# Performance work log

Hardware: AMD Instinct MI355X
Metric: run time of the kernel (lower is better)

## Reference

```python
import jax, jax.numpy as jnp
import numpy as np

EPS = 1e-12  # torch F.normalize eps

def _normalize(x):
    n = jnp.sqrt(jnp.sum(x * x, axis=-1, keepdims=True))
    return x / jnp.maximum(n, EPS)

def bgs_extended(d6s):
    # d6s: [B, N, D, 3, 2] -> rotation [B, N, D, 3, 3] (columns b1,b2,b3)
    b1 = _normalize(d6s[..., :, 0])
    a2 = d6s[..., :, 1]
    dot = jnp.sum(b1 * a2, axis=-1, keepdims=True)
    b2 = _normalize(a2 - dot * b1)
    b3 = jnp.cross(b1, b2, axis=-1)
    return jnp.stack([b1, b2, b3], axis=-1)

def setup_inputs() -> dict:
    key = jax.random.key(0)
    k1, k2, k3, k4, k5 = jax.random.split(key, 5)
    B, N, D, F = 8, 8192, 64, 64
    X = jax.random.normal(k1, (B, N, D, 3), dtype=jnp.float32)
    J = jax.random.normal(k2, (B, N, D, 3, 2), dtype=jnp.float32)
    A = jax.random.normal(k3, (F, D), dtype=jnp.float32)
    Bm = jax.random.normal(k4, (F, D), dtype=jnp.float32)
    C = jax.random.normal(k5, (F, D), dtype=jnp.float32)
    return {"X": X, "J": J, "A": A, "Bm": Bm, "C": C}

def reference(X, J, A, Bm, C):
    R = bgs_extended(J)  # [B,N,D,3,3]
    # RT_i X = dot(column i of R, X) -> compute all three at once: [B,N,D,3]
    RTX = jnp.einsum('bndki,bndk->bndi', R, X)
    rt0, rt1, rt2 = RTX[..., 0:1], RTX[..., 1:2], RTX[..., 2:3]
    # get_rrtx(i, R, s) == R[..., :, i] * s
    a_term = R[..., :, 0] * rt0 + R[..., :, 1] * rt1
    b_term = R[..., :, 1] * rt0 - R[..., :, 0] * rt1
    c_term = R[..., :, 2] * rt2
    Y = (jnp.einsum('fe,bnei->bnfi', A, a_term)
         + jnp.einsum('fe,bnei->bnfi', Bm, b_term)
         + jnp.einsum('fe,bnei->bnfi', C, c_term))
    return Y
```

## Files before the change

kernel.cpp:

```cpp
#include <hip/hip_runtime.h>

typedef __bf16 bf16;
typedef bf16 bf16x8 __attribute__((ext_vector_type(8)));
typedef float f32x4 __attribute__((ext_vector_type(4)));
typedef unsigned int u32;

#define PTS 16
#define WREG 6144

__device__ __forceinline__ void gld_lds16(const void* g, void* l) {
    __builtin_amdgcn_global_load_lds(
        (const __attribute__((address_space(1))) u32*)g,
        (__attribute__((address_space(3))) u32*)l, 16, 0, 0);
}

__global__ __launch_bounds__(256, 6)
void affine_linear_fused(const float* __restrict__ X, const float* __restrict__ J,
                         const float* __restrict__ A, const float* __restrict__ Bm,
                         const float* __restrict__ C, float* __restrict__ Y)
{
    __shared__ __attribute__((aligned(128))) unsigned char lds[4 * WREG];

    const int tid  = threadIdx.x;
    const int wave = tid >> 6;
    const int lane = tid & 63;
    const int l16  = lane & 15;
    const int lq   = lane >> 4;
    const long bn0 = (long)blockIdx.x * PTS;

    unsigned char* wbase = &lds[wave * WREG];

    {
        const float* jg = J + (bn0 + wave * 4) * 384;
        #pragma unroll
        for (int t = 0; t < 6; ++t)
            gld_lds16(jg + t * 256 + lane * 4, wbase + t * 1024);
    }

    float xv[4][3];
    {
        const float* xg = X + (bn0 + wave * 4) * 192 + lane * 3;
        #pragma unroll
        for (int q = 0; q < 4; ++q) {
            xv[q][0] = xg[q * 192 + 0];
            xv[q][1] = xg[q * 192 + 1];
            xv[q][2] = xg[q * 192 + 2];
        }
    }

    const int f = wave * 16 + l16;
    f32x4 wlo[6], whi[6];
    #pragma unroll
    for (int kk = 0; kk < 6; ++kk) {
        const float* src = (kk < 2) ? A : (kk < 4) ? Bm : C;
        const f32x4* p4 = (const f32x4*)(src + f * 64 + (kk & 1) * 32 + lq * 8);
        wlo[kk] = p4[0];
        whi[kk] = p4[1];
    }

    __asm__ volatile("s_waitcnt vmcnt(0)" ::: "memory");

    bf16x8 wfrag[6];
    #pragma unroll
    for (int kk = 0; kk < 6; ++kk) {
        bf16x8 w;
        w[0] = (bf16)wlo[kk][0]; w[1] = (bf16)wlo[kk][1];
        w[2] = (bf16)wlo[kk][2]; w[3] = (bf16)wlo[kk][3];
        w[4] = (bf16)whi[kk][0]; w[5] = (bf16)whi[kk][1];
        w[6] = (bf16)whi[kk][2]; w[7] = (bf16)whi[kk][3];
        wfrag[kk] = w;
    }

    const float* jlds = (const float*)wbase;
    #pragma unroll
    for (int q = 0; q < 4; ++q) {
        const float* jp = jlds + q * 384 + lane * 6;
        float2 ja  = *(const float2*)(jp + 0);
        float2 jb  = *(const float2*)(jp + 2);
        float2 jc2 = *(const float2*)(jp + 4);
        float a1x = ja.x,  a2x = ja.y;
        float a1y = jb.x,  a2y = jb.y;
        float a1z = jc2.x, a2z = jc2.y;
        float xx = xv[q][0], xy = xv[q][1], xz = xv[q][2];

        float n1sq = a1x*a1x + a1y*a1y + a1z*a1z;
        float inv1 = __builtin_amdgcn_rsqf(fmaxf(n1sq, 1e-24f));
        float b1x = a1x*inv1, b1y = a1y*inv1, b1z = a1z*inv1;
        float dot = b1x*a2x + b1y*a2y + b1z*a2z;
        float ux = a2x - dot*b1x, uy = a2y - dot*b1y, uz = a2z - dot*b1z;
        float n2sq = ux*ux + uy*uy + uz*uz;
        float inv2 = __builtin_amdgcn_rsqf(fmaxf(n2sq, 1e-24f));
        float b2x = ux*inv2, b2y = uy*inv2, b2z = uz*inv2;
        float b3x = b1y*b2z - b1z*b2y;
        float b3y = b1z*b2x - b1x*b2z;
        float b3z = b1x*b2y - b1y*b2x;

        float rt0 = b1x*xx + b1y*xy + b1z*xz;
        float rt1 = b2x*xx + b2y*xy + b2z*xz;
        float rt2 = b3x*xx + b3y*xy + b3z*xz;

        float at0 = b1x*rt0 + b2x*rt1;
        float at1 = b1y*rt0 + b2y*rt1;
        float at2 = b1z*rt0 + b2z*rt1;
        float bt0 = b2x*rt0 - b1x*rt1;
        float bt1 = b2y*rt0 - b1y*rt1;
        float bt2 = b2z*rt0 - b1z*rt1;
        float ct0 = b3x*rt2, ct1 = b3y*rt2, ct2 = b3z*rt2;

        bf16* r0 = (bf16*)(wbase + (q*3 + 0) * 400);
        bf16* r1 = (bf16*)(wbase + (q*3 + 1) * 400);
        bf16* r2 = (bf16*)(wbase + (q*3 + 2) * 400);
        r0[lane] = (bf16)at0; r0[64+lane] = (bf16)bt0; r0[128+lane] = (bf16)ct0;
        r1[lane] = (bf16)at1; r1[64+lane] = (bf16)bt1; r1[128+lane] = (bf16)ct1;
        r2[lane] = (bf16)at2; r2[64+lane] = (bf16)bt2; r2[128+lane] = (bf16)ct2;
    }

    __asm__ volatile("s_waitcnt lgkmcnt(0)" ::: "memory");
    __builtin_amdgcn_s_barrier();

    const unsigned char* arow[3];
    #pragma unroll
    for (int mt = 0; mt < 3; ++mt) {
        int m  = mt * 16 + l16;
        int wv = m / 12;
        int r  = m - wv * 12;
        arow[mt] = &lds[wv * WREG + r * 400] + lq * 16;
    }
    f32x4 acc[3];
    #pragma unroll
    for (int mt = 0; mt < 3; ++mt) acc[mt] = (f32x4){0.f, 0.f, 0.f, 0.f};
    #pragma unroll
    for (int kk = 0; kk < 6; ++kk) {
        #pragma unroll
        for (int mt = 0; mt < 3; ++mt) {
            bf16x8 af = *(const bf16x8*)(arow[mt] + kk * 64);
            acc[mt] = __builtin_amdgcn_mfma_f32_16x16x32_bf16(af, wfrag[kk], acc[mt], 0, 0, 0);
        }
    }

    __asm__ volatile("s_waitcnt lgkmcnt(0)" ::: "memory");
    __builtin_amdgcn_s_barrier();

    float* yw = (float*)wbase;
    #pragma unroll
    for (int mt = 0; mt < 3; ++mt) {
        #pragma unroll
        for (int r = 0; r < 4; ++r) {
            int m  = mt * 16 + lq * 4 + r;
            int wv = m / 12;
            int rr = m - wv * 12;
            int q  = rr / 3;
            int i  = rr - q * 3;
            int p  = wv * 4 + q;
            yw[p * 48 + l16 * 3 + i] = acc[mt][r];
        }
    }

    const f32x4* ysrc = (const f32x4*)yw;
    #pragma unroll
    for (int v = 0; v < 3; ++v) {
        int vi = v * 64 + lane;
        int p  = vi / 12;
        int vo = vi - p * 12;
        f32x4* dst = (f32x4*)(Y + (bn0 + p) * 192 + wave * 48) + vo;
        *dst = ysrc[vi];
    }
}

extern "C" void kernel_launch(void* const* d_in, const int* in_sizes, int n_in,
                              void* d_out, int out_size, void* d_ws, size_t ws_size,
                              hipStream_t stream) {
    const float* X  = (const float*)d_in[0];
    const float* J  = (const float*)d_in[1];
    const float* A  = (const float*)d_in[2];
    const float* Bm = (const float*)d_in[3];
    const float* C  = (const float*)d_in[4];
    float* Y = (float*)d_out;

    const int points = in_sizes[0] / (64 * 3);
    const int blocks = points / PTS;
    affine_linear_fused<<<blocks, 256, 0, stream>>>(X, J, A, Bm, C, Y);
}
```

Before: 205.8 us.

## Load J into registers and store Y directly, dropping LDS staging

J is now read with per-lane float2 global loads straight into registers instead of async global-to-LDS copies. The output is written directly from the MFMA accumulators to global memory with scalar strided stores, replacing the LDS transpose followed by 16-byte vector stores. This removes a barrier and shrinks the per-wave LDS region, and the launch-bounds occupancy hint drops from 6 to 4. In exchange, the global stores are narrower and less well coalesced, and the J loads are less contiguous per lane.

```diff
diff --git a/kernel.cpp b/kernel.cpp
--- a/kernel.cpp
+++ b/kernel.cpp
@@ -3,18 +3,11 @@
 typedef __bf16 bf16;
 typedef bf16 bf16x8 __attribute__((ext_vector_type(8)));
 typedef float f32x4 __attribute__((ext_vector_type(4)));
-typedef unsigned int u32;
 
 #define PTS 16
-#define WREG 6144
+#define WREG 4800
 
-__device__ __forceinline__ void gld_lds16(const void* g, void* l) {
-    __builtin_amdgcn_global_load_lds(
-        (const __attribute__((address_space(1))) u32*)g,
-        (__attribute__((address_space(3))) u32*)l, 16, 0, 0);
-}
-
-__global__ __launch_bounds__(256, 6)
+__global__ __launch_bounds__(256, 4)
 void affine_linear_fused(const float* __restrict__ X, const float* __restrict__ J,
                          const float* __restrict__ A, const float* __restrict__ Bm,
                          const float* __restrict__ C, float* __restrict__ Y)
@@ -30,11 +23,18 @@
 
     unsigned char* wbase = &lds[wave * WREG];
 
+    float jv[4][6];
     {
-        const float* jg = J + (bn0 + wave * 4) * 384;
+        const float* jg = J + (bn0 + wave * 4) * 384 + lane * 6;
         #pragma unroll
-        for (int t = 0; t < 6; ++t)
-            gld_lds16(jg + t * 256 + lane * 4, wbase + t * 1024);
+        for (int q = 0; q < 4; ++q) {
+            float2 ja  = *(const float2*)(jg + q * 384 + 0);
+            float2 jb  = *(const float2*)(jg + q * 384 + 2);
+            float2 jc2 = *(const float2*)(jg + q * 384 + 4);
+            jv[q][0] = ja.x;  jv[q][1] = ja.y;
+            jv[q][2] = jb.x;  jv[q][3] = jb.y;
+            jv[q][4] = jc2.x; jv[q][5] = jc2.y;
+        }
     }
 
     float xv[4][3];
@@ -71,16 +71,11 @@
         wfrag[kk] = w;
     }
 
-    const float* jlds = (const float*)wbase;
     #pragma unroll
     for (int q = 0; q < 4; ++q) {
-        const float* jp = jlds + q * 384 + lane * 6;
-        float2 ja  = *(const float2*)(jp + 0);
-        float2 jb  = *(const float2*)(jp + 2);
-        float2 jc2 = *(const float2*)(jp + 4);
-        float a1x = ja.x,  a2x = ja.y;
-        float a1y = jb.x,  a2y = jb.y;
-        float a1z = jc2.x, a2z = jc2.y;
+        float a1x = jv[q][0], a2x = jv[q][1];
+        float a1y = jv[q][2], a2y = jv[q][3];
+        float a1z = jv[q][4], a2z = jv[q][5];
         float xx = xv[q][0], xy = xv[q][1], xz = xv[q][2];
 
         float n1sq = a1x*a1x + a1y*a1y + a1z*a1z;
@@ -115,8 +110,7 @@
         r2[lane] = (bf16)at2; r2[64+lane] = (bf16)bt2; r2[128+lane] = (bf16)ct2;
     }
 
-    __asm__ volatile("s_waitcnt lgkmcnt(0)" ::: "memory");
-    __builtin_amdgcn_s_barrier();
+    __syncthreads();
 
     const unsigned char* arow[3];
     #pragma unroll
@@ -138,32 +132,16 @@
         }
     }
 
-    __asm__ volatile("s_waitcnt lgkmcnt(0)" ::: "memory");
-    __builtin_amdgcn_s_barrier();
-
-    float* yw = (float*)wbase;
+    float* yb = Y + (bn0) * 192 + f * 3;
     #pragma unroll
     for (int mt = 0; mt < 3; ++mt) {
         #pragma unroll
         for (int r = 0; r < 4; ++r) {
-            int m  = mt * 16 + lq * 4 + r;
-            int wv = m / 12;
-            int rr = m - wv * 12;
-            int q  = rr / 3;
-            int i  = rr - q * 3;
-            int p  = wv * 4 + q;
-            yw[p * 48 + l16 * 3 + i] = acc[mt][r];
+            int m = mt * 16 + lq * 4 + r;
+            int p = m / 3;
+            int i = m - p * 3;
+            yb[p * 192 + i] = acc[mt][r];
         }
-    }
-
-    const f32x4* ysrc = (const f32x4*)yw;
-    #pragma unroll
-    for (int v = 0; v < 3; ++v) {
-        int vi = v * 64 + lane;
-        int p  = vi / 12;
-        int vo = vi - p * 12;
-        f32x4* dst = (f32x4*)(Y + (bn0 + p) * 192 + wave * 48) + vo;
-        *dst = ysrc[vi];
     }
 }
 
```

After: 207.5 us. No clear change (+0.8%).
